# Optimization experiments

Measured on AMD Instinct MI355X. Metric: run time of the kernel, lower is better.

The kernel has to match this reference:

```python
import jax, jax.numpy as jnp
import numpy as np

N, D, H, B = 16384, 256, 4, 64
K_EDGE, TOP_K, NUM_HOPS = 3, 5, 2
EDGE_THRESH = 0.3
EPS = 1e-8


def setup_inputs() -> dict:
    key = jax.random.key(0)
    ks = jax.random.split(key, 32)
    g = lambda i, shape, sc=1.0: jax.random.normal(ks[i], shape, jnp.float32) * sc
    # sparse-ish symmetric adjacency (avg ~33 nonzeros/row, like a pruned memory graph)
    adj = jax.random.uniform(ks[0], (N, N), jnp.float32)
    adj = adj * (jax.random.uniform(ks[1], (N, N), jnp.float32) < 0.002)
    adj = jnp.maximum(adj, adj.T)
    return dict(
        nodes=g(2, (N, D)),
        node_values=g(3, (N,)),
        adjacency=adj,
        related_pos=g(4, (B, D)),
        query=g(5, (B, D)),
        w_in=g(6, (3 * D, D), D ** -0.5),
        b_in=jnp.zeros((3 * D,), jnp.float32),
        w_out=g(7, (D, D), D ** -0.5),
        b_out=jnp.zeros((D,), jnp.float32),
        rel_w1=g(8, (2 * D, D), (2 * D) ** -0.5),
        rel_b1=jnp.zeros((D,), jnp.float32),
        rel_w2=g(9, (D, D // 2), D ** -0.5),
        rel_b2=jnp.zeros((D // 2,), jnp.float32),
        rel_w3=g(10, (D // 2, 1), (D // 2) ** -0.5),
        rel_b3=jnp.zeros((1,), jnp.float32),
        gru_w_ih=g(11, (3 * D, D), D ** -0.5),
        gru_w_hh=g(12, (3 * D, D), D ** -0.5),
        gru_b_ih=jnp.zeros((3 * D,), jnp.float32),
        gru_b_hh=jnp.zeros((3 * D,), jnp.float32),
        node_timestamps=jax.random.randint(ks[13], (N,), 0, N),
        write_idx=jax.random.randint(ks[14], (B,), 0, N),
        total_writes=N,
    )


def _l2n(x):
    return x / (jnp.linalg.norm(x, axis=-1, keepdims=True) + EPS)


def reference(nodes, node_values, adjacency, related_pos, query,
              w_in, b_in, w_out, b_out,
              rel_w1, rel_b1, rel_w2, rel_b2, rel_w3, rel_b3,
              gru_w_ih, gru_w_hh, gru_b_ih, gru_b_hh,
              node_timestamps, write_idx, total_writes):
    b, d = query.shape
    n = nodes.shape[0]
    dh = d // H
    nodes_n = _l2n(nodes)

    # ---- write path: cosine-sim top-k edge scoring + relation-encoder MLP ----
    sims_w = _l2n(related_pos) @ nodes_n.T                      # [B,N]
    _, nbr = jax.lax.top_k(sims_w, K_EDGE)                      # [B,K]
    src = nodes[write_idx]                                      # [B,D]
    dst = nodes[nbr]                                            # [B,K,D]
    comb = jnp.concatenate(
        [jnp.broadcast_to(src[:, None, :], dst.shape), dst], -1)  # [B,K,2D]
    h = jax.nn.relu(comb @ rel_w1 + rel_b1)
    h = jax.nn.relu(h @ rel_w2 + rel_b2)
    strength = jax.nn.sigmoid(h @ rel_w3 + rel_b3)[..., 0]     # [B,K]
    same = nbr == write_idx[:, None]
    old = adjacency[write_idx[:, None], nbr]
    val = jnp.where(same, old, strength)                        # skip self-edges
    adj2 = adjacency.at[write_idx[:, None], nbr].set(val)
    adj2 = adj2.at[nbr, write_idx[:, None]].set(val)            # symmetric write

    # ---- retrieval: weighted cosine similarity + top-k seeds ----
    sims = _l2n(query) @ nodes_n.T                              # [B,N]
    recency = jnp.exp(-0.01 * (total_writes - node_timestamps).astype(jnp.float32))
    weighted = sims * jax.nn.sigmoid(node_values) * recency
    _, seed = jax.lax.top_k(weighted, TOP_K)                    # [B,TOP_K]
    visited = jnp.zeros((b, n), bool).at[jnp.arange(b)[:, None], seed].set(True)

    # ---- multi-hop graph expansion over thresholded adjacency ----
    adj_bool = (adj2 > EDGE_THRESH).astype(jnp.float32)
    for _ in range(NUM_HOPS):
        visited = visited | ((visited.astype(jnp.float32) @ adj_bool) > 0)

    # ---- masked multi-head attention: query attends to visited nodes ----
    q = (query @ w_in[:d].T + b_in[:d]).reshape(b, H, dh)
    k = (nodes @ w_in[d:2 * d].T + b_in[d:2 * d]).reshape(n, H, dh)
    v = (nodes @ w_in[2 * d:].T + b_in[2 * d:]).reshape(n, H, dh)
    scores = jnp.einsum('bhd,nhd->bhn', q, k) / np.float32(np.sqrt(dh))
    scores = jnp.where(visited[:, None, :], scores, jnp.float32(-1e9))
    attn = jax.nn.softmax(scores, axis=-1)
    ctx = jnp.einsum('bhn,nhd->bhd', attn, v).reshape(b, d)
    attended = ctx @ w_out.T + b_out                            # [B,D]

    # ---- GRUCell memory evolution: x=query, h=attended ----
    gi = query @ gru_w_ih.T + gru_b_ih
    gh = attended @ gru_w_hh.T + gru_b_hh
    i_r, i_z, i_n = jnp.split(gi, 3, -1)
    h_r, h_z, h_n = jnp.split(gh, 3, -1)
    r = jax.nn.sigmoid(i_r + h_r)
    z = jax.nn.sigmoid(i_z + h_z)
    nn_ = jnp.tanh(i_n + r * h_n)
    evolved = (1.0 - z) * nn_ + z * attended                    # [B,D]
    return evolved
```

## Files before the change

### kernel.cpp

```cpp
#include <hip/hip_runtime.h>
#include <math.h>
#include <stdint.h>

#define NN 16384
#define DD 256
#define ETH 0.3f
#define EDGE_CAP (4*1024*1024)

typedef unsigned long long u64;
typedef uint32_t u32;
typedef float f32x4 __attribute__((ext_vector_type(4)));

__global__ __launch_bounds__(256) void node_stats_k(const float* __restrict__ nodes,
    const float* __restrict__ nv, const int* __restrict__ ts, const int* __restrict__ tw,
    float* __restrict__ inv_norm, float* __restrict__ sal){
  int row = blockIdx.x*4 + (threadIdx.x>>6);
  int lane = threadIdx.x & 63;
  const float4* r4 = (const float4*)(nodes + (size_t)row*DD);
  float4 v = r4[lane];
  float s = v.x*v.x+v.y*v.y+v.z*v.z+v.w*v.w;
  #pragma unroll
  for (int o=32;o>0;o>>=1) s += __shfl_down(s,o);
  if (lane==0){
    inv_norm[row] = 1.0f/(sqrtf(s)+1e-8f);
    float x = nv[row];
    float sig = 1.0f/(1.0f+expf(-x));
    float rec = expf(-0.01f*(float)(tw[0]-ts[row]));
    sal[row] = sig*rec;
  }
}

__global__ __launch_bounds__(64) void norm_qr_k(const float* __restrict__ query,
    const float* __restrict__ related, float* __restrict__ qr){
  int blk = blockIdx.x; int lane = threadIdx.x;
  const float* src = (blk<64)? (related + (size_t)blk*DD) : (query + (size_t)(blk-64)*DD);
  float4 v = ((const float4*)src)[lane];
  float s = v.x*v.x+v.y*v.y+v.z*v.z+v.w*v.w;
  #pragma unroll
  for (int o=32;o>0;o>>=1) s += __shfl_down(s,o);
  s = __shfl(s,0);
  float inv = 1.0f/(sqrtf(s)+1e-8f);
  ((float4*)(qr + (size_t)blk*DD))[lane] = make_float4(v.x*inv,v.y*inv,v.z*inv,v.w*inv);
}

#define ACC8(r) do{ \
    accA[r].x += qs*nv0.x; accA[r].y += qs*nv0.y; accA[r].z += qs*nv0.z; accA[r].w += qs*nv0.w; \
    accB[r].x += qs*nv1.x; accB[r].y += qs*nv1.y; accB[r].z += qs*nv1.z; accB[r].w += qs*nv1.w; }while(0)

template<int RM>
__global__ __launch_bounds__(256) void gemm_smallM_k(const float* __restrict__ Qm,
    const float* __restrict__ nodes, float* __restrict__ out0, float* __restrict__ out1,
    const float* __restrict__ inv_norm, const float* __restrict__ sal, int mode){
  constexpr int M = RM*32;
  constexpr int KC = 32;
  __shared__ float qk[KC*M];
  __shared__ float ndk[KC*64];
  int t = threadIdx.x;
  int qg = t>>3, ng = t&7;
  int n0 = blockIdx.x*64;
  float4 accA[RM], accB[RM];
  #pragma unroll
  for (int r=0;r<RM;r++){ accA[r]=make_float4(0,0,0,0); accB[r]=make_float4(0,0,0,0); }
  for (int kb=0; kb<DD; kb+=KC){
    if (t < M){
      const float4* src = (const float4*)(Qm + (size_t)t*DD + kb);
      #pragma unroll
      for (int i=0;i<KC/4;i++){
        float4 w = src[i];
        qk[(i*4+0)*M+t]=w.x; qk[(i*4+1)*M+t]=w.y;
        qk[(i*4+2)*M+t]=w.z; qk[(i*4+3)*M+t]=w.w;
      }
    }
    {
      int nn = t&63, kq = t>>6;
      const float4* src = (const float4*)(nodes + (size_t)(n0+nn)*DD + kb + kq*8);
      float4 a = src[0], b = src[1];
      ndk[(kq*8+0)*64+nn]=a.x; ndk[(kq*8+1)*64+nn]=a.y; ndk[(kq*8+2)*64+nn]=a.z; ndk[(kq*8+3)*64+nn]=a.w;
      ndk[(kq*8+4)*64+nn]=b.x; ndk[(kq*8+5)*64+nn]=b.y; ndk[(kq*8+6)*64+nn]=b.z; ndk[(kq*8+7)*64+nn]=b.w;
    }
    __syncthreads();
    for (int k=0;k<KC;k++){
      float4 nv0 = *(const float4*)&ndk[k*64 + ng*8];
      float4 nv1 = *(const float4*)&ndk[k*64 + ng*8 + 4];
      float4 q0  = *(const float4*)&qk[k*M + qg*RM];
      float qs;
      qs=q0.x; ACC8(0); qs=q0.y; ACC8(1); qs=q0.z; ACC8(2); qs=q0.w; ACC8(3);
      if constexpr (RM==8){
        float4 q1 = *(const float4*)&qk[k*M + qg*RM + 4];
        qs=q1.x; ACC8(4); qs=q1.y; ACC8(5); qs=q1.z; ACC8(6); qs=q1.w; ACC8(7);
      }
    }
    __syncthreads();
  }
  int nbase = n0 + ng*8;
  float4 in0, in1, sa0, sa1;
  if (mode==0){
    in0 = *(const float4*)&inv_norm[nbase]; in1 = *(const float4*)&inv_norm[nbase+4];
    sa0 = *(const float4*)&sal[nbase];      sa1 = *(const float4*)&sal[nbase+4];
  }
  #pragma unroll
  for (int r=0;r<RM;r++){
    int row = qg*RM + r;
    float4 a = accA[r], b = accB[r];
    if (mode==0){
      float4 s0 = make_float4(a.x*in0.x, a.y*in0.y, a.z*in0.z, a.w*in0.w);
      float4 s1 = make_float4(b.x*in1.x, b.y*in1.y, b.z*in1.z, b.w*in1.w);
      if (row < 64){
        *(float4*)&out0[(size_t)row*NN + nbase]     = s0;
        *(float4*)&out0[(size_t)row*NN + nbase + 4] = s1;
      } else {
        float4 w0 = make_float4(s0.x*sa0.x, s0.y*sa0.y, s0.z*sa0.z, s0.w*sa0.w);
        float4 w1 = make_float4(s1.x*sa1.x, s1.y*sa1.y, s1.z*sa1.z, s1.w*sa1.w);
        *(float4*)&out1[(size_t)(row-64)*NN + nbase]     = w0;
        *(float4*)&out1[(size_t)(row-64)*NN + nbase + 4] = w1;
      }
    } else {
      float4 s0 = make_float4(a.x*0.125f, a.y*0.125f, a.z*0.125f, a.w*0.125f);
      float4 s1 = make_float4(b.x*0.125f, b.y*0.125f, b.z*0.125f, b.w*0.125f);
      *(float4*)&out0[(size_t)row*NN + nbase]     = s0;
      *(float4*)&out0[(size_t)row*NN + nbase + 4] = s1;
    }
  }
}

#define TK_INS(cv,ci) do{ \
  if (cv>v4 || (cv==v4 && ci<i4)){ \
    if (cv>v0 || (cv==v0 && ci<i0)){ v4=v3;i4=i3; v3=v2;i3=i2; v2=v1;i2=i1; v1=v0;i1=i0; v0=cv;i0=ci; } \
    else if (cv>v1 || (cv==v1 && ci<i1)){ v4=v3;i4=i3; v3=v2;i3=i2; v2=v1;i2=i1; v1=cv;i1=ci; } \
    else if (cv>v2 || (cv==v2 && ci<i2)){ v4=v3;i4=i3; v3=v2;i3=i2; v2=cv;i2=ci; } \
    else if (cv>v3 || (cv==v3 && ci<i3)){ v4=v3;i4=i3; v3=cv;i3=ci; } \
    else { v4=cv;i4=ci; } \
  } \
}while(0)

__global__ __launch_bounds__(1024) void topk_k(const float* __restrict__ src, int K,
    int* __restrict__ outIdx, u64* __restrict__ vis){
  int b = blockIdx.x, t = threadIdx.x;
  const float* row = src + (size_t)b*NN;
  float v0=-3.0e38f,v1=-3.0e38f,v2=-3.0e38f,v3=-3.0e38f,v4=-3.0e38f;
  int i0=0x7fffffff,i1=0x7fffffff,i2=0x7fffffff,i3=0x7fffffff,i4=0x7fffffff;
  for (int n=t; n<NN; n+=1024){
    float cv = row[n];
    TK_INS(cv, n);
  }
  __shared__ float sv[1024*5];
  __shared__ int   si[1024*5];
  sv[t*5+0]=v0; si[t*5+0]=i0; sv[t*5+1]=v1; si[t*5+1]=i1;
  sv[t*5+2]=v2; si[t*5+2]=i2; sv[t*5+3]=v3; si[t*5+3]=i3;
  sv[t*5+4]=v4; si[t*5+4]=i4;
  __syncthreads();
  for (int s=512; s>0; s>>=1){
    if (t < s){
      #pragma unroll
      for (int k=0;k<5;k++){
        float cv = sv[(t+s)*5+k]; int ci = si[(t+s)*5+k];
        TK_INS(cv, ci);
      }
      sv[t*5+0]=v0; si[t*5+0]=i0; sv[t*5+1]=v1; si[t*5+1]=i1;
      sv[t*5+2]=v2; si[t*5+2]=i2; sv[t*5+3]=v3; si[t*5+3]=i3;
      sv[t*5+4]=v4; si[t*5+4]=i4;
    }
    __syncthreads();
  }
  if (t==0){
    int idxs[5] = {i0,i1,i2,i3,i4};
    for (int kk=0; kk<K; kk++){
      outIdx[b*K+kk] = idxs[kk];
      if (vis) atomicOr(&vis[idxs[kk]], 1ull<<b);
    }
  }
}

__global__ __launch_bounds__(256) void rel_patch_k(const float* __restrict__ nodes,
    const int* __restrict__ write_idx, const int* __restrict__ nbr,
    const float* __restrict__ w1, const float* __restrict__ b1,
    const float* __restrict__ w2, const float* __restrict__ b2,
    const float* __restrict__ w3, const float* __restrict__ b3,
    u32* __restrict__ modkeys, u32* __restrict__ addkeys, int* __restrict__ ctrl,
    u32* __restrict__ rowmod){
  int b = blockIdx.x, t = threadIdx.x;
  __shared__ float comb[512], h1[256], red[128];
  int w = write_idx[b];
  for (int k=0;k<3;k++){
    int nb = nbr[b*3+k];
    comb[t]     = nodes[(size_t)w*DD + t];
    comb[256+t] = nodes[(size_t)nb*DD + t];
    __syncthreads();
    float a1 = b1[t];
    for (int i=0;i<512;i++) a1 += comb[i]*w1[(size_t)i*256 + t];
    h1[t] = a1>0.f ? a1 : 0.f;
    __syncthreads();
    if (t<128){
      float a2 = b2[t];
      for (int i=0;i<256;i++) a2 += h1[i]*w2[(size_t)i*128 + t];
      float h2 = a2>0.f ? a2 : 0.f;
      red[t] = h2*w3[t];
    }
    __syncthreads();
    for (int s=64;s>0;s>>=1){ if (t<s) red[t]+=red[t+s]; __syncthreads(); }
    if (t==0 && nb != w){
      float strength = 1.0f/(1.0f+expf(-(red[0]+b3[0])));
      u32 k1 = ((u32)w<<14)|(u32)nb, k2 = ((u32)nb<<14)|(u32)w;
      int m = atomicAdd(&ctrl[1],2);
      modkeys[m]=k1; modkeys[m+1]=k2;
      if (strength > ETH){ int a=atomicAdd(&ctrl[2],2); addkeys[a]=k1; addkeys[a+1]=k2; }
      atomicOr(&rowmod[(u32)w>>5], 1u<<((u32)w&31));
      atomicOr(&rowmod[(u32)nb>>5], 1u<<((u32)nb&31));
    }
    __syncthreads();
  }
}

#define LCAP 4096
#define GITER 8
#define ISSUE(P, GB) do{ \
  asm volatile("global_load_dwordx4 %0, %1, off" : "=v"(P##0) : "v"(a4 + tid + (size_t)((GB)+0)*stride)); \
  asm volatile("global_load_dwordx4 %0, %1, off" : "=v"(P##1) : "v"(a4 + tid + (size_t)((GB)+1)*stride)); \
  asm volatile("global_load_dwordx4 %0, %1, off" : "=v"(P##2) : "v"(a4 + tid + (size_t)((GB)+2)*stride)); \
  asm volatile("global_load_dwordx4 %0, %1, off" : "=v"(P##3) : "v"(a4 + tid + (size_t)((GB)+3)*stride)); \
  asm volatile("global_load_dwordx4 %0, %1, off" : "=v"(P##4) : "v"(a4 + tid + (size_t)((GB)+4)*stride)); \
  asm volatile("global_load_dwordx4 %0, %1, off" : "=v"(P##5) : "v"(a4 + tid + (size_t)((GB)+5)*stride)); \
  asm volatile("global_load_dwordx4 %0, %1, off" : "=v"(P##6) : "v"(a4 + tid + (size_t)((GB)+6)*stride)); \
  asm volatile("global_load_dwordx4 %0, %1, off" : "=v"(P##7) : "v"(a4 + tid + (size_t)((GB)+7)*stride)); \
}while(0)
#define PROC1(XX, GI) do{ \
  _Pragma("unroll") \
  for (int e=0;e<4;e++){ \
    if (XX[e] > ETH){ \
      size_t li = (tid + (size_t)(GI)*stride)*4 + e; \
      u32 i = (u32)(li >> 14), j = (u32)(li & 16383); \
      u32 key = (i<<14)|j; \
      bool keep = true; \
      if ((rowmod[i>>5]>>(i&31))&1u){ \
        for (int c=0;c<nm;c++) if (modkeys[c]==key){ keep=false; break; } \
      } \
      if (keep){ \
        int p = atomicAdd(&lcnt, 1); \
        if (p < LCAP) lbuf[p] = key; \
        else { int d = atomicAdd(ecnt,1); if (d < EDGE_CAP) edges[d] = key; } \
      } \
    } \
  } }while(0)
#define PROC8(P, GB) do{ \
  PROC1(P##0,(GB)+0); PROC1(P##1,(GB)+1); PROC1(P##2,(GB)+2); PROC1(P##3,(GB)+3); \
  PROC1(P##4,(GB)+4); PROC1(P##5,(GB)+5); PROC1(P##6,(GB)+6); PROC1(P##7,(GB)+7); \
}while(0)

__global__ __launch_bounds__(256) void scan_adj_k(const float* __restrict__ adj,
    const u32* __restrict__ rowmod, const u32* __restrict__ modkeys,
    const int* __restrict__ ctrl, u32* __restrict__ edges, int* __restrict__ ecnt){
  __shared__ u32 lbuf[LCAP];
  __shared__ int lcnt, gbase;
  int t = threadIdx.x;
  if (t==0) lcnt = 0;
  __syncthreads();
  int nm = ctrl[1];
  size_t tid = (size_t)blockIdx.x*256 + t;
  size_t stride = (size_t)gridDim.x*256;
  const f32x4* a4 = (const f32x4*)adj;
  const size_t total4 = (size_t)NN*NN/4;
  const int iters = (int)(total4 / stride);
  f32x4 xa0,xa1,xa2,xa3,xa4,xa5,xa6,xa7;
  f32x4 xb0,xb1,xb2,xb3,xb4,xb5,xb6,xb7;
  ISSUE(xa, 0);
  #pragma unroll 1
  for (int g=0; g<iters; g+=2*GITER){
    ISSUE(xb, g+GITER);
    asm volatile("s_waitcnt vmcnt(8)" ::: "memory");
    __builtin_amdgcn_sched_barrier(0);
    PROC8(xa, g);
    if (g + 2*GITER < iters){
      ISSUE(xa, g+2*GITER);
      asm volatile("s_waitcnt vmcnt(8)" ::: "memory");
    } else {
      asm volatile("s_waitcnt vmcnt(0)" ::: "memory");
    }
    __builtin_amdgcn_sched_barrier(0);
    PROC8(xb, g+GITER);
  }
  __syncthreads();
  int cnt = lcnt; if (cnt > LCAP) cnt = LCAP;
  if (cnt > 0){
    if (t==0) gbase = atomicAdd(ecnt, cnt);
    __syncthreads();
    int b0 = gbase;
    for (int i=t; i<cnt; i+=256){
      int d = b0 + i;
      if (d < EDGE_CAP) edges[d] = lbuf[i];
    }
  }
}

__global__ void patch_add_k(const u32* __restrict__ addkeys, const int* __restrict__ ctrl,
    u32* __restrict__ edges, int* __restrict__ ecnt){
  if (blockIdx.x==0 && threadIdx.x==0){
    int na = ctrl[2];
    int base = atomicAdd(ecnt, na);
    for (int i=0;i<na;i++) if (base+i < EDGE_CAP) edges[base+i] = addkeys[i];
  }
}

__global__ __launch_bounds__(256) void propagate_k(const u32* __restrict__ edges,
    const int* __restrict__ ecnt, const u64* __restrict__ vin, u64* __restrict__ vout){
  int n = *ecnt; if (n > EDGE_CAP) n = EDGE_CAP;
  int tid = blockIdx.x*256 + threadIdx.x;
  int stride = gridDim.x*256;
  for (int idx=tid; idx<n; idx+=stride){
    u32 key = edges[idx];
    u32 i = key>>14, j = key & 16383u;
    u64 wv = vin[i];
    if (wv) atomicOr(&vout[j], wv);
  }
}

__global__ __launch_bounds__(256) void qproj_k(const float* __restrict__ query,
    const float* __restrict__ w_in, const float* __restrict__ b_in, float* __restrict__ qproj){
  int b = blockIdx.x, o = threadIdx.x;
  float s = b_in[o];
  const float* wr = w_in + (size_t)o*256;
  const float* q = query + (size_t)b*256;
  for (int c=0;c<256;c++) s += q[c]*wr[c];
  qproj[b*256+o]=s;
}

__global__ __launch_bounds__(256) void qw_k(const float* __restrict__ qproj,
    const float* __restrict__ w_in, float* __restrict__ qW){
  int r = blockIdx.x;
  int c = threadIdx.x;
  int b = r>>2, hh = r&3;
  float s=0.f;
  for (int dh=0; dh<64; dh++)
    s += qproj[b*256 + hh*64 + dh] * w_in[(size_t)(256 + hh*64 + dh)*256 + c];
  qW[(size_t)r*256+c]=s;
}

__global__ __launch_bounds__(256) void agg_k(const float* __restrict__ scores,
    const u64* __restrict__ vis, const float* __restrict__ nodes,
    float* __restrict__ partial, float* __restrict__ m_arr, float* __restrict__ s_arr){
  int c = blockIdx.x;
  int h = blockIdx.y;
  int t = threadIdx.x;
  int bb = t >> 2, qq = t & 3;
  __shared__ float att[64][257];
  int n0 = c*256;
  for (int idx=t; idx<64*256; idx+=256){
    int rb = idx>>8, nn = idx&255;
    int node = n0 + nn;
    float raw = scores[((size_t)(rb*4+h))*NN + node];
    att[rb][nn] = ((vis[node]>>rb)&1ull) ? raw : -3.0e38f;
  }
  __syncthreads();
  float m = -3.0e38f;
  for (int j=0;j<64;j++) m = fmaxf(m, att[bb][qq*64+j]);
  m = fmaxf(m, __shfl_xor(m,1));
  m = fmaxf(m, __shfl_xor(m,2));
  float s = 0.f;
  for (int j=0;j<64;j++){ float v = att[bb][qq*64+j]; if (v > -1.0e37f) s += __expf(v-m); }
  s += __shfl_xor(s,1);
  s += __shfl_xor(s,2);
  __syncthreads();
  for (int j=0;j<64;j++){
    float v = att[bb][qq*64+j];
    att[bb][qq*64+j] = (v > -1.0e37f) ? __expf(v-m) : 0.f;
  }
  __syncthreads();
  float4 acc[16];
  #pragma unroll
  for (int i=0;i<16;i++) acc[i] = make_float4(0.f,0.f,0.f,0.f);
  for (int nn=0; nn<256; nn++){
    float a = att[bb][nn];
    if (a != 0.f){
      const float4* nr = (const float4*)(nodes + ((size_t)(n0+nn))*DD + qq*64);
      #pragma unroll
      for (int i=0;i<16;i++){
        float4 x = nr[i];
        acc[i].x += a*x.x; acc[i].y += a*x.y; acc[i].z += a*x.z; acc[i].w += a*x.w;
      }
    }
  }
  float* dst = partial + (((size_t)(c*4+h)*64 + bb)*256) + qq*64;
  #pragma unroll
  for (int i=0;i<16;i++) ((float4*)dst)[i] = acc[i];
  if (qq==0){
    m_arr[(c*4+h)*64 + bb] = m;
    s_arr[(c*4+h)*64 + bb] = s;
  }
}

__global__ __launch_bounds__(256) void reduce_partial_k(const float* __restrict__ partial,
    const float* __restrict__ m_arr, const float* __restrict__ s_arr,
    float* __restrict__ ctxraw){
  int idx = blockIdx.x*256 + threadIdx.x;
  int d = idx & 255; int bh = idx >> 8;
  int hh = bh & 3, b = bh >> 2;
  float M = -3.0e38f, S = 0.f, acc = 0.f;
  for (int c=0;c<64;c++){
    int rb = (c*4+hh)*64 + b;
    float mc = m_arr[rb], sc = s_arr[rb];
    float pv = partial[((size_t)rb)*256 + d];
    if (mc > M){
      float w = __expf(M - mc);
      acc = acc*w + pv;
      S   = S*w + sc;
      M   = mc;
    } else {
      float w = __expf(mc - M);
      acc += pv*w;
      S   += sc*w;
    }
  }
  ctxraw[idx] = acc / S;
}

__global__ __launch_bounds__(256) void ctx_k(const float* __restrict__ ctxraw,
    const float* __restrict__ w_in, const float* __restrict__ b_in, float* __restrict__ ctx){
  int b = blockIdx.x, o = threadIdx.x;
  int hh = o >> 6;
  const float* cr = ctxraw + (size_t)(b*4+hh)*256;
  const float* wr = w_in + (size_t)(512+o)*256;
  float s = b_in[512+o];
  for (int d=0; d<256; d++) s += cr[d]*wr[d];
  ctx[b*256+o] = s;
}

__global__ __launch_bounds__(256) void attended_k(const float* __restrict__ ctx,
    const float* __restrict__ w_out, const float* __restrict__ b_out, float* __restrict__ att){
  int b = blockIdx.x, o = threadIdx.x;
  const float* cr = ctx + (size_t)b*256;
  const float* wr = w_out + (size_t)o*256;
  float s = b_out[o];
  for (int c=0;c<256;c++) s += cr[c]*wr[c];
  att[b*256+o] = s;
}

__global__ __launch_bounds__(256) void gru_k(const float* __restrict__ query,
    const float* __restrict__ att, const float* __restrict__ w_ih, const float* __restrict__ w_hh,
    const float* __restrict__ b_ih, const float* __restrict__ b_hh, float* __restrict__ out){
  int b = blockIdx.x, o = threadIdx.x;
  const float* q = query + (size_t)b*256;
  const float* a = att + (size_t)b*256;
  float ir=b_ih[o], iz=b_ih[256+o], inn=b_ih[512+o];
  float hr=b_hh[o], hz=b_hh[256+o], hn=b_hh[512+o];
  for (int c=0;c<256;c++){
    float qc=q[c], ac=a[c];
    ir += qc*w_ih[(size_t)o*256+c];
    iz += qc*w_ih[(size_t)(256+o)*256+c];
    inn+= qc*w_ih[(size_t)(512+o)*256+c];
    hr += ac*w_hh[(size_t)o*256+c];
    hz += ac*w_hh[(size_t)(256+o)*256+c];
    hn += ac*w_hh[(size_t)(512+o)*256+c];
  }
  float r = 1.f/(1.f+expf(-(ir+hr)));
  float z = 1.f/(1.f+expf(-(iz+hz)));
  float nval = tanhf(inn + r*hn);
  out[b*256+o] = (1.f-z)*nval + z*a[o];
}

extern "C" void kernel_launch(void* const* d_in, const int* in_sizes, int n_in,
                              void* d_out, int out_size, void* d_ws, size_t ws_size,
                              hipStream_t stream){
  (void)in_sizes; (void)n_in; (void)out_size; (void)ws_size;
  const float* nodes     = (const float*)d_in[0];
  const float* node_vals = (const float*)d_in[1];
  const float* adjacency = (const float*)d_in[2];
  const float* related   = (const float*)d_in[3];
  const float* query     = (const float*)d_in[4];
  const float* w_in      = (const float*)d_in[5];
  const float* b_in      = (const float*)d_in[6];
  const float* w_out     = (const float*)d_in[7];
  const float* b_out     = (const float*)d_in[8];
  const float* rel_w1    = (const float*)d_in[9];
  const float* rel_b1    = (const float*)d_in[10];
  const float* rel_w2    = (const float*)d_in[11];
  const float* rel_b2    = (const float*)d_in[12];
  const float* rel_w3    = (const float*)d_in[13];
  const float* rel_b3    = (const float*)d_in[14];
  const float* gw_ih     = (const float*)d_in[15];
  const float* gw_hh     = (const float*)d_in[16];
  const float* gb_ih     = (const float*)d_in[17];
  const float* gb_hh     = (const float*)d_in[18];
  const int*   ts        = (const int*)d_in[19];
  const int*   write_idx = (const int*)d_in[20];
  const int*   tw        = (const int*)d_in[21];
  float* out = (float*)d_out;

  char* ws = (char*)d_ws;
  size_t off = 0;
  auto alloc = [&](size_t bytes)->char*{
    char* p = ws + off; off += (bytes + 255) & ~(size_t)255; return p;
  };
  float* inv_norm = (float*)alloc(NN*4);
  float* sal      = (float*)alloc(NN*4);
  float* qr       = (float*)alloc(128*DD*4);
  float* simw     = (float*)alloc((size_t)64*NN*4);
  float* wsims    = (float*)alloc((size_t)64*NN*4);
  int*   nbr      = (int*)  alloc(64*3*4);
  int*   seed     = (int*)  alloc(64*5*4);
  float* qproj    = (float*)alloc(64*256*4);
  float* qW       = (float*)alloc(256*256*4);
  float* scores   = (float*)alloc((size_t)256*NN*4);
  float* m_arr    = (float*)alloc(64*4*64*4);
  float* s_arr    = (float*)alloc(64*4*64*4);
  float* ctxraw   = (float*)alloc(64*4*256*4);
  float* ctx      = (float*)alloc(64*256*4);
  float* attended = (float*)alloc(64*256*4);
  u64*   V0       = (u64*)  alloc(NN*8);
  u64*   V1       = (u64*)  alloc(NN*8);
  u32*   edges    = (u32*)  alloc((size_t)EDGE_CAP*4);
  float* partial  = (float*)edges;
  int*   ctrl     = (int*)  alloc(256);
  u32*   modkeys  = (u32*)  alloc(512*4);
  u32*   addkeys  = (u32*)  alloc(512*4);
  u32*   rowmod   = (u32*)  alloc(NN/8);

  hipMemsetAsync(ctrl, 0, 256, stream);
  hipMemsetAsync(rowmod, 0, NN/8, stream);
  hipMemsetAsync(V0, 0, NN*8, stream);

  node_stats_k<<<NN/4, 256, 0, stream>>>(nodes, node_vals, ts, tw, inv_norm, sal);
  norm_qr_k<<<128, 64, 0, stream>>>(query, related, qr);
  gemm_smallM_k<4><<<NN/64, 256, 0, stream>>>(qr, nodes, simw, wsims, inv_norm, sal, 0);
  topk_k<<<64, 1024, 0, stream>>>(simw, 3, nbr, (u64*)nullptr);
  topk_k<<<64, 1024, 0, stream>>>(wsims, 5, seed, V0);
  rel_patch_k<<<64, 256, 0, stream>>>(nodes, write_idx, nbr, rel_w1, rel_b1, rel_w2, rel_b2,
                                      rel_w3, rel_b3, modkeys, addkeys, ctrl, rowmod);
  scan_adj_k<<<2048, 256, 0, stream>>>(adjacency, rowmod, modkeys, ctrl, edges, &ctrl[0]);
  patch_add_k<<<1, 64, 0, stream>>>(addkeys, ctrl, edges, &ctrl[0]);
  hipMemcpyAsync(V1, V0, NN*8, hipMemcpyDeviceToDevice, stream);
  propagate_k<<<1024, 256, 0, stream>>>(edges, &ctrl[0], V0, V1);
  hipMemcpyAsync(V0, V1, NN*8, hipMemcpyDeviceToDevice, stream);
  propagate_k<<<1024, 256, 0, stream>>>(edges, &ctrl[0], V1, V0);
  qproj_k<<<64, 256, 0, stream>>>(query, w_in, b_in, qproj);
  qw_k<<<256, 256, 0, stream>>>(qproj, w_in, qW);
  gemm_smallM_k<8><<<NN/64, 256, 0, stream>>>(qW, nodes, scores, (float*)nullptr,
                                              (const float*)nullptr, (const float*)nullptr, 1);
  agg_k<<<dim3(64,4), 256, 0, stream>>>(scores, V0, nodes, partial, m_arr, s_arr);
  reduce_partial_k<<<256, 256, 0, stream>>>(partial, m_arr, s_arr, ctxraw);
  ctx_k<<<64, 256, 0, stream>>>(ctxraw, w_in, b_in, ctx);
  attended_k<<<64, 256, 0, stream>>>(ctx, w_out, b_out, attended);
  gru_k<<<64, 256, 0, stream>>>(query, attended, gw_ih, gw_hh, gb_ih, gb_hh, out);
}
```

Baseline: 1.265 ms.

## Fuse first hop propagation into adjacency scan and merge tail kernels

The first graph-propagation hop now runs inside the adjacency scan and the add-patch kernel, removing one propagate pass over the edge list. The adjacency loads get a non-temporal hint. The two query projection kernels become one, and the partial reduction, ctx projection, output projection and GRU are fused into a single per-batch kernel. This cuts launches and intermediate buffers, but the fused tail runs on only 64 blocks, so its reduction has less parallelism than the separate 256-block kernel it replaces.

```diff
diff --git a/kernel.cpp b/kernel.cpp
--- a/kernel.cpp
+++ b/kernel.cpp
@@ -214,14 +214,14 @@
 #define LCAP 4096
 #define GITER 8
 #define ISSUE(P, GB) do{ \
-  asm volatile("global_load_dwordx4 %0, %1, off" : "=v"(P##0) : "v"(a4 + tid + (size_t)((GB)+0)*stride)); \
-  asm volatile("global_load_dwordx4 %0, %1, off" : "=v"(P##1) : "v"(a4 + tid + (size_t)((GB)+1)*stride)); \
-  asm volatile("global_load_dwordx4 %0, %1, off" : "=v"(P##2) : "v"(a4 + tid + (size_t)((GB)+2)*stride)); \
-  asm volatile("global_load_dwordx4 %0, %1, off" : "=v"(P##3) : "v"(a4 + tid + (size_t)((GB)+3)*stride)); \
-  asm volatile("global_load_dwordx4 %0, %1, off" : "=v"(P##4) : "v"(a4 + tid + (size_t)((GB)+4)*stride)); \
-  asm volatile("global_load_dwordx4 %0, %1, off" : "=v"(P##5) : "v"(a4 + tid + (size_t)((GB)+5)*stride)); \
-  asm volatile("global_load_dwordx4 %0, %1, off" : "=v"(P##6) : "v"(a4 + tid + (size_t)((GB)+6)*stride)); \
-  asm volatile("global_load_dwordx4 %0, %1, off" : "=v"(P##7) : "v"(a4 + tid + (size_t)((GB)+7)*stride)); \
+  asm volatile("global_load_dwordx4 %0, %1, off nt" : "=v"(P##0) : "v"(a4 + tid + (size_t)((GB)+0)*stride)); \
+  asm volatile("global_load_dwordx4 %0, %1, off nt" : "=v"(P##1) : "v"(a4 + tid + (size_t)((GB)+1)*stride)); \
+  asm volatile("global_load_dwordx4 %0, %1, off nt" : "=v"(P##2) : "v"(a4 + tid + (size_t)((GB)+2)*stride)); \
+  asm volatile("global_load_dwordx4 %0, %1, off nt" : "=v"(P##3) : "v"(a4 + tid + (size_t)((GB)+3)*stride)); \
+  asm volatile("global_load_dwordx4 %0, %1, off nt" : "=v"(P##4) : "v"(a4 + tid + (size_t)((GB)+4)*stride)); \
+  asm volatile("global_load_dwordx4 %0, %1, off nt" : "=v"(P##5) : "v"(a4 + tid + (size_t)((GB)+5)*stride)); \
+  asm volatile("global_load_dwordx4 %0, %1, off nt" : "=v"(P##6) : "v"(a4 + tid + (size_t)((GB)+6)*stride)); \
+  asm volatile("global_load_dwordx4 %0, %1, off nt" : "=v"(P##7) : "v"(a4 + tid + (size_t)((GB)+7)*stride)); \
 }while(0)
 #define PROC1(XX, GI) do{ \
   _Pragma("unroll") \
@@ -235,6 +235,8 @@
         for (int c=0;c<nm;c++) if (modkeys[c]==key){ keep=false; break; } \
       } \
       if (keep){ \
+        u64 wv = vseed[i]; \
+        if (wv) atomicOr(&vout[j], wv); \
         int p = atomicAdd(&lcnt, 1); \
         if (p < LCAP) lbuf[p] = key; \
         else { int d = atomicAdd(ecnt,1); if (d < EDGE_CAP) edges[d] = key; } \
@@ -248,7 +250,8 @@
 
 __global__ __launch_bounds__(256) void scan_adj_k(const float* __restrict__ adj,
     const u32* __restrict__ rowmod, const u32* __restrict__ modkeys,
-    const int* __restrict__ ctrl, u32* __restrict__ edges, int* __restrict__ ecnt){
+    const int* __restrict__ ctrl, u32* __restrict__ edges, int* __restrict__ ecnt,
+    const u64* __restrict__ vseed, u64* __restrict__ vout){
   __shared__ u32 lbuf[LCAP];
   __shared__ int lcnt, gbase;
   int t = threadIdx.x;
@@ -292,11 +295,18 @@
 }
 
 __global__ void patch_add_k(const u32* __restrict__ addkeys, const int* __restrict__ ctrl,
-    u32* __restrict__ edges, int* __restrict__ ecnt){
+    u32* __restrict__ edges, int* __restrict__ ecnt,
+    const u64* __restrict__ vseed, u64* __restrict__ vout){
   if (blockIdx.x==0 && threadIdx.x==0){
     int na = ctrl[2];
     int base = atomicAdd(ecnt, na);
-    for (int i=0;i<na;i++) if (base+i < EDGE_CAP) edges[base+i] = addkeys[i];
+    for (int i=0;i<na;i++){
+      u32 key = addkeys[i];
+      if (base+i < EDGE_CAP) edges[base+i] = key;
+      u32 ii = key>>14, jj = key & 16383u;
+      u64 wv = vseed[ii];
+      if (wv) atomicOr(&vout[jj], wv);
+    }
   }
 }
 
@@ -313,25 +323,24 @@
   }
 }
 
-__global__ __launch_bounds__(256) void qproj_k(const float* __restrict__ query,
-    const float* __restrict__ w_in, const float* __restrict__ b_in, float* __restrict__ qproj){
-  int b = blockIdx.x, o = threadIdx.x;
-  float s = b_in[o];
-  const float* wr = w_in + (size_t)o*256;
-  const float* q = query + (size_t)b*256;
-  for (int c=0;c<256;c++) s += q[c]*wr[c];
-  qproj[b*256+o]=s;
-}
-
-__global__ __launch_bounds__(256) void qw_k(const float* __restrict__ qproj,
-    const float* __restrict__ w_in, float* __restrict__ qW){
-  int r = blockIdx.x;
-  int c = threadIdx.x;
-  int b = r>>2, hh = r&3;
-  float s=0.f;
-  for (int dh=0; dh<64; dh++)
-    s += qproj[b*256 + hh*64 + dh] * w_in[(size_t)(256 + hh*64 + dh)*256 + c];
-  qW[(size_t)r*256+c]=s;
+__global__ __launch_bounds__(256) void qprojw_k(const float* __restrict__ query,
+    const float* __restrict__ w_in, const float* __restrict__ b_in, float* __restrict__ qW){
+  int b = blockIdx.x, t = threadIdx.x;
+  __shared__ float q_l[256], qp[256];
+  q_l[t] = query[(size_t)b*256 + t];
+  __syncthreads();
+  float s = b_in[t];
+  const float* wr = w_in + (size_t)t*256;
+  for (int c=0;c<256;c++) s += q_l[c]*wr[c];
+  qp[t] = s;
+  __syncthreads();
+  #pragma unroll
+  for (int h=0; h<4; h++){
+    float acc = 0.f;
+    for (int dh=0; dh<64; dh++)
+      acc += qp[h*64+dh] * w_in[(size_t)(256 + h*64 + dh)*256 + t];
+    qW[(size_t)(b*4+h)*256 + t] = acc;
+  }
 }
 
 __global__ __launch_bounds__(256) void agg_k(const float* __restrict__ scores,
@@ -387,73 +396,74 @@
   }
 }
 
-__global__ __launch_bounds__(256) void reduce_partial_k(const float* __restrict__ partial,
+__global__ __launch_bounds__(256) void tail_k(const float* __restrict__ partial,
     const float* __restrict__ m_arr, const float* __restrict__ s_arr,
-    float* __restrict__ ctxraw){
-  int idx = blockIdx.x*256 + threadIdx.x;
-  int d = idx & 255; int bh = idx >> 8;
-  int hh = bh & 3, b = bh >> 2;
-  float M = -3.0e38f, S = 0.f, acc = 0.f;
-  for (int c=0;c<64;c++){
-    int rb = (c*4+hh)*64 + b;
-    float mc = m_arr[rb], sc = s_arr[rb];
-    float pv = partial[((size_t)rb)*256 + d];
-    if (mc > M){
-      float w = __expf(M - mc);
-      acc = acc*w + pv;
-      S   = S*w + sc;
-      M   = mc;
-    } else {
-      float w = __expf(mc - M);
-      acc += pv*w;
-      S   += sc*w;
-    }
-  }
-  ctxraw[idx] = acc / S;
-}
-
-__global__ __launch_bounds__(256) void ctx_k(const float* __restrict__ ctxraw,
-    const float* __restrict__ w_in, const float* __restrict__ b_in, float* __restrict__ ctx){
-  int b = blockIdx.x, o = threadIdx.x;
-  int hh = o >> 6;
-  const float* cr = ctxraw + (size_t)(b*4+hh)*256;
-  const float* wr = w_in + (size_t)(512+o)*256;
-  float s = b_in[512+o];
-  for (int d=0; d<256; d++) s += cr[d]*wr[d];
-  ctx[b*256+o] = s;
-}
-
-__global__ __launch_bounds__(256) void attended_k(const float* __restrict__ ctx,
-    const float* __restrict__ w_out, const float* __restrict__ b_out, float* __restrict__ att){
-  int b = blockIdx.x, o = threadIdx.x;
-  const float* cr = ctx + (size_t)b*256;
-  const float* wr = w_out + (size_t)o*256;
-  float s = b_out[o];
-  for (int c=0;c<256;c++) s += cr[c]*wr[c];
-  att[b*256+o] = s;
-}
-
-__global__ __launch_bounds__(256) void gru_k(const float* __restrict__ query,
-    const float* __restrict__ att, const float* __restrict__ w_ih, const float* __restrict__ w_hh,
-    const float* __restrict__ b_ih, const float* __restrict__ b_hh, float* __restrict__ out){
-  int b = blockIdx.x, o = threadIdx.x;
-  const float* q = query + (size_t)b*256;
-  const float* a = att + (size_t)b*256;
-  float ir=b_ih[o], iz=b_ih[256+o], inn=b_ih[512+o];
-  float hr=b_hh[o], hz=b_hh[256+o], hn=b_hh[512+o];
-  for (int c=0;c<256;c++){
-    float qc=q[c], ac=a[c];
-    ir += qc*w_ih[(size_t)o*256+c];
-    iz += qc*w_ih[(size_t)(256+o)*256+c];
-    inn+= qc*w_ih[(size_t)(512+o)*256+c];
-    hr += ac*w_hh[(size_t)o*256+c];
-    hz += ac*w_hh[(size_t)(256+o)*256+c];
-    hn += ac*w_hh[(size_t)(512+o)*256+c];
-  }
-  float r = 1.f/(1.f+expf(-(ir+hr)));
-  float z = 1.f/(1.f+expf(-(iz+hz)));
-  float nval = tanhf(inn + r*hn);
-  out[b*256+o] = (1.f-z)*nval + z*a[o];
+    const float* __restrict__ w_in, const float* __restrict__ b_in,
+    const float* __restrict__ w_out, const float* __restrict__ b_out,
+    const float* __restrict__ query,
+    const float* __restrict__ w_ih, const float* __restrict__ w_hh,
+    const float* __restrict__ b_ih, const float* __restrict__ b_hh,
+    float* __restrict__ out){
+  int b = blockIdx.x, t = threadIdx.x;
+  __shared__ float lm[256], ls[256];
+  __shared__ float cr[4][256];
+  __shared__ float cx[256], at[256];
+  lm[t] = m_arr[t*64 + b];
+  ls[t] = s_arr[t*64 + b];
+  __syncthreads();
+  #pragma unroll
+  for (int h=0; h<4; h++){
+    float M = -3.0e38f, S = 0.f, acc = 0.f;
+    for (int c=0; c<64; c++){
+      float mc = lm[c*4+h], sc = ls[c*4+h];
+      float pv = partial[((size_t)((c*4+h)*64 + b))*256 + t];
+      if (mc > M){
+        float w = __expf(M - mc);
+        acc = acc*w + pv;
+        S   = S*w + sc;
+        M   = mc;
+      } else {
+        float w = __expf(mc - M);
+        acc += pv*w;
+        S   += sc*w;
+      }
+    }
+    cr[h][t] = acc / S;
+  }
+  __syncthreads();
+  {
+    int hh = t >> 6;
+    const float* wr = w_in + (size_t)(512+t)*256;
+    float s = b_in[512+t];
+    for (int d=0; d<256; d++) s += cr[hh][d]*wr[d];
+    cx[t] = s;
+  }
+  __syncthreads();
+  {
+    const float* wr = w_out + (size_t)t*256;
+    float s = b_out[t];
+    for (int c=0;c<256;c++) s += cx[c]*wr[c];
+    at[t] = s;
+  }
+  __syncthreads();
+  {
+    const float* q = query + (size_t)b*256;
+    float ir=b_ih[t], iz=b_ih[256+t], inn=b_ih[512+t];
+    float hr=b_hh[t], hz=b_hh[256+t], hn=b_hh[512+t];
+    for (int c=0;c<256;c++){
+      float qc=q[c], ac=at[c];
+      ir += qc*w_ih[(size_t)t*256+c];
+      iz += qc*w_ih[(size_t)(256+t)*256+c];
+      inn+= qc*w_ih[(size_t)(512+t)*256+c];
+      hr += ac*w_hh[(size_t)t*256+c];
+      hz += ac*w_hh[(size_t)(256+t)*256+c];
+      hn += ac*w_hh[(size_t)(512+t)*256+c];
+    }
+    float r = 1.f/(1.f+expf(-(ir+hr)));
+    float z = 1.f/(1.f+expf(-(iz+hz)));
+    float nval = tanhf(inn + r*hn);
+    out[(size_t)b*256+t] = (1.f-z)*nval + z*at[t];
+  }
 }
 
 extern "C" void kernel_launch(void* const* d_in, const int* in_sizes, int n_in,
@@ -496,14 +506,10 @@
   float* wsims    = (float*)alloc((size_t)64*NN*4);
   int*   nbr      = (int*)  alloc(64*3*4);
   int*   seed     = (int*)  alloc(64*5*4);
-  float* qproj    = (float*)alloc(64*256*4);
   float* qW       = (float*)alloc(256*256*4);
   float* scores   = (float*)alloc((size_t)256*NN*4);
   float* m_arr    = (float*)alloc(64*4*64*4);
   float* s_arr    = (float*)alloc(64*4*64*4);
-  float* ctxraw   = (float*)alloc(64*4*256*4);
-  float* ctx      = (float*)alloc(64*256*4);
-  float* attended = (float*)alloc(64*256*4);
   u64*   V0       = (u64*)  alloc(NN*8);
   u64*   V1       = (u64*)  alloc(NN*8);
   u32*   edges    = (u32*)  alloc((size_t)EDGE_CAP*4);
@@ -524,19 +530,15 @@
   topk_k<<<64, 1024, 0, stream>>>(wsims, 5, seed, V0);
   rel_patch_k<<<64, 256, 0, stream>>>(nodes, write_idx, nbr, rel_w1, rel_b1, rel_w2, rel_b2,
                                       rel_w3, rel_b3, modkeys, addkeys, ctrl, rowmod);
-  scan_adj_k<<<2048, 256, 0, stream>>>(adjacency, rowmod, modkeys, ctrl, edges, &ctrl[0]);
-  patch_add_k<<<1, 64, 0, stream>>>(addkeys, ctrl, edges, &ctrl[0]);
   hipMemcpyAsync(V1, V0, NN*8, hipMemcpyDeviceToDevice, stream);
-  propagate_k<<<1024, 256, 0, stream>>>(edges, &ctrl[0], V0, V1);
+  scan_adj_k<<<2048, 256, 0, stream>>>(adjacency, rowmod, modkeys, ctrl, edges, &ctrl[0], V0, V1);
+  patch_add_k<<<1, 64, 0, stream>>>(addkeys, ctrl, edges, &ctrl[0], V0, V1);
   hipMemcpyAsync(V0, V1, NN*8, hipMemcpyDeviceToDevice, stream);
   propagate_k<<<1024, 256, 0, stream>>>(edges, &ctrl[0], V1, V0);
-  qproj_k<<<64, 256, 0, stream>>>(query, w_in, b_in, qproj);
-  qw_k<<<256, 256, 0, stream>>>(qproj, w_in, qW);
+  qprojw_k<<<64, 256, 0, stream>>>(query, w_in, b_in, qW);
   gemm_smallM_k<8><<<NN/64, 256, 0, stream>>>(qW, nodes, scores, (float*)nullptr,
                                               (const float*)nullptr, (const float*)nullptr, 1);
   agg_k<<<dim3(64,4), 256, 0, stream>>>(scores, V0, nodes, partial, m_arr, s_arr);
-  reduce_partial_k<<<256, 256, 0, stream>>>(partial, m_arr, s_arr, ctxraw);
-  ctx_k<<<64, 256, 0, stream>>>(ctxraw, w_in, b_in, ctx);
-  attended_k<<<64, 256, 0, stream>>>(ctx, w_out, b_out, attended);
-  gru_k<<<64, 256, 0, stream>>>(query, attended, gw_ih, gw_hh, gb_ih, gb_hh, out);
-}
+  tail_k<<<64, 256, 0, stream>>>(partial, m_arr, s_arr, w_in, b_in, w_out, b_out,
+                                 query, gw_ih, gw_hh, gb_ih, gb_hh, out);
+}
```

After: 1.343 ms. 1.06x slower.
